# Kernel tuning notes

Measured on AMD Instinct MI355X. Metric: run time of the kernel, lower is better.

The kernel has to match this reference:

```python
import jax, jax.numpy as jnp
import numpy as np

N, E, B = 100000, 400000, 2048     # nodes, edges, graphs
H, L = 300, 5                      # hidden_feats, n_layers
NT, EF, T = 120, 16, 128           # num_node_types, in_edge_feats, n_tasks
EPS = 1e-5                         # BatchNorm eps (eval mode, running_mean=0, running_var=1)


def setup_inputs() -> dict:
    key = jax.random.key(0)
    ks = jax.random.split(key, 16)
    g = lambda i, shape, s=0.05: jax.random.normal(ks[i], shape, jnp.float32) * s
    return dict(
        node_types=jax.random.randint(ks[0], (N,), 0, NT),
        src=jax.random.randint(ks[1], (E,), 0, N),
        dst=jax.random.randint(ks[2], (E,), 0, N),
        graph_ids=jnp.sort(jax.random.randint(ks[3], (N,), 0, B)),
        edge_feats=jax.random.normal(ks[4], (E, EF), jnp.float32),
        node_emb=g(5, (NT, H), 1.0),          # nn.Embedding(num_node_types, H)
        Wn=g(6, (L, H, H)), bn=g(7, (L, H), 0.01),      # per-layer node projection
        We=g(8, (L, EF, H)), be=g(9, (L, H), 0.01),     # per-layer edge projection
        root=g(10, (L, H)),                   # per-layer root embedding (Embedding(1,H))
        gamma=1.0 + g(11, (L, H), 0.01), beta=g(12, (L, H), 0.01),  # layer BN
        vn_emb=g(13, (H,)),                   # virtual node embedding (Embedding(1,H))
        W1=g(14, (L - 1, H, 2 * H)), b1=jnp.zeros((L - 1, 2 * H), jnp.float32),
        g1=jnp.ones((L - 1, 2 * H), jnp.float32), be1=jnp.zeros((L - 1, 2 * H), jnp.float32),
        W2=g(15, (L - 1, 2 * H, H)), b2=jnp.zeros((L - 1, H), jnp.float32),
        g2=jnp.ones((L - 1, H), jnp.float32), be2=jnp.zeros((L - 1, H), jnp.float32),
        pW=jax.random.normal(jax.random.fold_in(key, 99), (H, T), jnp.float32) * 0.05,
        pb=jnp.zeros((T,), jnp.float32),
    )


def _bn(x, ga, be_):
    # eval-mode BatchNorm1d with running_mean=0, running_var=1
    return x * (ga / jnp.sqrt(1.0 + EPS)) + be_


def reference(node_types, src, dst, graph_ids, edge_feats, node_emb,
              Wn, bn, We, be, root, gamma, beta, vn_emb,
              W1, b1, g1, be1, W2, b2, g2, be2, pW, pb):
    ones_e = jnp.ones((E,), jnp.float32)
    deg = jax.ops.segment_sum(ones_e, dst, num_segments=N) + 1.0   # in_degrees + 1
    norm = deg ** -0.5
    edge_norm = (norm[src] * norm[dst])[:, None]                   # (E, 1)
    inv_deg = (1.0 / deg)[:, None]                                 # (N, 1)

    h = node_emb[node_types]                      # (N, H) node encoder
    vn = jnp.broadcast_to(vn_emb, (B, H))         # (B, H) virtual node feats

    for l in range(L):
        h = h + vn[graph_ids]                     # dgl.broadcast_nodes
        x = h @ Wn[l] + bn[l]                     # (N, H)
        e = edge_feats @ We[l] + be[l]            # (E, H)
        m = edge_norm * jax.nn.relu(x[src] + e)   # per-edge messages
        agg = jax.ops.segment_sum(m, dst, num_segments=N)          # (N, H)
        out = agg + jax.nn.relu(x + root[l]) * inv_deg
        out = _bn(out, gamma[l], beta[l])
        if l != L - 1:
            out = jax.nn.relu(out)
        h_in = h                                  # h_list[l] (after vn broadcast add)
        h = out                                   # dropout p=0 -> identity; residual=False
        if l < L - 1:
            vtmp = jax.ops.segment_sum(h_in, graph_ids, num_segments=B) + vn
            z = jax.nn.relu(_bn(vtmp @ W1[l] + b1[l], g1[l], be1[l]))
            vn = jax.nn.relu(_bn(z @ W2[l] + b2[l], g2[l], be2[l]))

    # mean readout over each graph, then linear head
    counts = jax.ops.segment_sum(jnp.ones((N,), jnp.float32), graph_ids, num_segments=B)
    gsum = jax.ops.segment_sum(h, graph_ids, num_segments=B)
    gmean = gsum / jnp.maximum(counts, 1.0)[:, None]
    return gmean @ pW + pb                        # (B, n_tasks)
```

## Files before the change

### kernel.cpp

```cpp
#include <hip/hip_runtime.h>
#include <hip/hip_bf16.h>
#include <hip/hip_fp16.h>

#define N_ 100000
#define MPAD 100096
#define E_ 400000
#define B_ 2048
#define H_ 300
#define KP_ 320
#define L_ 5
#define EF_ 16
#define T_ 128
#define ANODES 4
#define EMAX 96
#define BNS 0.9999950000374997f

typedef unsigned short ushort_t;
typedef short bf16x8 __attribute__((ext_vector_type(8)));
typedef float f32x4 __attribute__((ext_vector_type(4)));

__device__ __forceinline__ ushort_t f2b(float v) {
    unsigned u = __float_as_uint(v);
    unsigned r = (u + 0x7FFFu + ((u >> 16) & 1u)) >> 16;
    return (ushort_t)r;
}

__device__ __forceinline__ float b2f(ushort_t u) {
    return __uint_as_float(((unsigned)u) << 16);
}

__device__ __forceinline__ void gl_lds16(const void* g, void* l) {
    __builtin_amdgcn_global_load_lds(
        (const __attribute__((address_space(1))) void*)g,
        (__attribute__((address_space(3))) void*)l, 16, 0, 0);
}

__device__ __forceinline__ int swzcol(int r, int j) {
    int u = ((j >> 3) & 3) ^ ((r >> 1) & 3);
    return (j & ~31) | (u << 3) | (j & 7);
}

__global__ void k_hist(const int* __restrict__ dst, int* __restrict__ degi, int E) {
    int e = blockIdx.x * blockDim.x + threadIdx.x;
    if (e < E) atomicAdd(&degi[dst[e]], 1);
}

__global__ void k_norm(const int* __restrict__ degi, float* __restrict__ nrm,
                       float* __restrict__ invdeg, int N) {
    int n = blockIdx.x * blockDim.x + threadIdx.x;
    if (n < N) {
        float d = (float)degi[n] + 1.0f;
        nrm[n] = 1.0f / sqrtf(d);
        invdeg[n] = 1.0f / d;
    }
}

__global__ void k_scan1(const int* __restrict__ in, int* __restrict__ out,
                        int* __restrict__ partial, int N) {
    __shared__ int s[1024];
    int i = blockIdx.x * 1024 + threadIdx.x;
    int v = (i < N) ? in[i] : 0;
    s[threadIdx.x] = v;
    __syncthreads();
    for (int off = 1; off < 1024; off <<= 1) {
        int t = (threadIdx.x >= off) ? s[threadIdx.x - off] : 0;
        __syncthreads();
        s[threadIdx.x] += t;
        __syncthreads();
    }
    if (i < N) out[i] = s[threadIdx.x] - v;
    if (threadIdx.x == 1023) partial[blockIdx.x] = s[1023];
}

__global__ void k_scan2(int* __restrict__ partial, int nb, int* __restrict__ totalOut) {
    __shared__ int sh[128];
    int t = threadIdx.x;
    int v = (t < nb) ? partial[t] : 0;
    sh[t] = v;
    __syncthreads();
    for (int off = 1; off < 128; off <<= 1) {
        int u = (t >= off) ? sh[t - off] : 0;
        __syncthreads();
        sh[t] += u;
        __syncthreads();
    }
    if (t < nb) partial[t] = sh[t] - v;
    if (t == 127) *totalOut = sh[127];
}

__global__ void k_scan3(int* __restrict__ out, const int* __restrict__ partial, int N) {
    int i = blockIdx.x * 1024 + threadIdx.x;
    if (i < N) out[i] += partial[blockIdx.x];
}

__global__ void k_scatter(const int* __restrict__ dst, const int* __restrict__ src,
                          const float* __restrict__ ef, const float* __restrict__ nrm,
                          int* __restrict__ cursor, int* __restrict__ csrc_s,
                          ushort_t* __restrict__ ef16, float* __restrict__ en_csr, int E) {
    int e = blockIdx.x * blockDim.x + threadIdx.x;
    if (e >= E) return;
    int d = dst[e], s = src[e];
    int pos = atomicAdd(&cursor[d], 1);
    csrc_s[pos] = s * KP_;
    en_csr[pos] = nrm[s] * nrm[d];
    const float4* ep = (const float4*)&ef[(size_t)e * EF_];
    float4 e0 = ep[0], e1 = ep[1], e2 = ep[2], e3 = ep[3];
    uint4 ua, ub;
    ua.x = __builtin_bit_cast(unsigned, __floats2half2_rn(e0.x, e0.y));
    ua.y = __builtin_bit_cast(unsigned, __floats2half2_rn(e0.z, e0.w));
    ua.z = __builtin_bit_cast(unsigned, __floats2half2_rn(e1.x, e1.y));
    ua.w = __builtin_bit_cast(unsigned, __floats2half2_rn(e1.z, e1.w));
    ub.x = __builtin_bit_cast(unsigned, __floats2half2_rn(e2.x, e2.y));
    ub.y = __builtin_bit_cast(unsigned, __floats2half2_rn(e2.z, e2.w));
    ub.z = __builtin_bit_cast(unsigned, __floats2half2_rn(e3.x, e3.y));
    ub.w = __builtin_bit_cast(unsigned, __floats2half2_rn(e3.z, e3.w));
    uint4* op = (uint4*)&ef16[(size_t)pos * 16];
    op[0] = ua; op[1] = ub;
}

__global__ void k_rowstart(const int* __restrict__ gid, int* __restrict__ rs, int N, int B) {
    int b = blockIdx.x * blockDim.x + threadIdx.x;
    if (b <= B) {
        int lo = 0, hi = N;
        while (lo < hi) { int mid = (lo + hi) >> 1; if (gid[mid] < b) lo = mid + 1; else hi = mid; }
        rs[b] = lo;
    }
}

__global__ void k_hinit(const int* __restrict__ nt, const float* __restrict__ emb,
                        const float* __restrict__ vn_emb,
                        ushort_t* __restrict__ h_bf) {
    int n = blockIdx.x; int j = threadIdx.x;
    if (j >= KP_) return;
    float v = (j < H_) ? emb[(size_t)nt[n] * H_ + j] + vn_emb[j] : 0.f;
    h_bf[(size_t)n * KP_ + swzcol(n, j)] = f2b(v);
}

__global__ void k_vninit(const float* __restrict__ vn_emb, float* __restrict__ vn) {
    int b = blockIdx.x; int j = threadIdx.x;
    if (j >= H_) return;
    vn[(size_t)b * H_ + j] = vn_emb[j];
}

__global__ void k_convW(const float* __restrict__ W, ushort_t* __restrict__ WT,
                        int nl, int K, int Nout, int KPv, int NPBv) {
    int UPR = KPv / 8;
    int tot = nl * NPBv * UPR;
    int idx = blockIdx.x * 256 + threadIdx.x;
    if (idx >= tot) return;
    int l = idx / (NPBv * UPR); int r = idx % (NPBv * UPR);
    int n = r / UPR; int ku = r % UPR;
    int k0 = ku * 8;
    int swz = (ku & 3) ^ ((n >> 1) & 3);
    size_t d = ((size_t)l * NPBv + n) * KPv + (size_t)(k0 & ~31) + swz * 8;
    #pragma unroll
    for (int i = 0; i < 8; i++) {
        int k = k0 + i;
        float v = (k < K && n < Nout) ? W[((size_t)l * K + k) * Nout + n] : 0.f;
        WT[d + i] = f2b(v);
    }
}

__global__ void k_convWeh(const float* __restrict__ We, unsigned* __restrict__ Weh) {
    int idx = blockIdx.x * 256 + threadIdx.x;
    if (idx >= L_ * 8 * H_) return;
    int l = idx / (8 * H_); int r = idx % (8 * H_);
    int k2 = r / H_; int j = r % H_;
    float a = We[((size_t)l * EF_ + 2 * k2) * H_ + j];
    float b = We[((size_t)l * EF_ + 2 * k2 + 1) * H_ + j];
    Weh[((size_t)l * 8 + k2) * H_ + j] = __builtin_bit_cast(unsigned, __floats2half2_rn(a, b));
}

#define MB 128
#define NB 128
__launch_bounds__(256)
__global__ void k_bgemm(const ushort_t* __restrict__ A, const ushort_t* __restrict__ BT,
                        int M, int Nn, int KP,
                        const float* __restrict__ bias, const float* __restrict__ scale,
                        const float* __restrict__ shift, int relu,
                        float* __restrict__ Cf, int ldf,
                        ushort_t* __restrict__ Cb, int ldb, int swzout) {
    __shared__ ushort_t As[MB * 32];
    __shared__ ushort_t Bs[NB * 32];
    int tid = threadIdx.x;
    int lane = tid & 63, wid = tid >> 6;
    int wm = wid >> 1, wn = wid & 1;
    int m0 = blockIdx.x * MB, n0 = blockIdx.y * NB;
    f32x4 acc[4][4];
    #pragma unroll
    for (int mi = 0; mi < 4; mi++)
        #pragma unroll
        for (int ni = 0; ni < 4; ni++)
            acc[mi][ni] = (f32x4){0.f, 0.f, 0.f, 0.f};

    const ushort_t* Ab = A + (size_t)m0 * KP;
    const ushort_t* Bb = BT + (size_t)n0 * KP;
    int lr = lane & 15, lg = lane >> 4;

    for (int k0 = 0; k0 < KP; k0 += 32) {
        #pragma unroll
        for (int i = 0; i < 2; i++) {
            int li = tid + 256 * i;
            int r = li >> 2, u = li & 3;
            gl_lds16(Ab + (size_t)r * KP + k0 + u * 8, &As[(size_t)(li & ~63) * 8]);
        }
        #pragma unroll
        for (int i = 0; i < 2; i++) {
            int li = tid + 256 * i;
            int r = li >> 2, u = li & 3;
            gl_lds16(Bb + (size_t)r * KP + k0 + u * 8, &Bs[(size_t)(li & ~63) * 8]);
        }
        __syncthreads();
        bf16x8 af[4], bv[4];
        #pragma unroll
        for (int mi = 0; mi < 4; mi++) {
            int rr = wm * 64 + mi * 16 + lr;
            int uu = lg ^ ((rr >> 1) & 3);
            af[mi] = *(const bf16x8*)&As[rr * 32 + uu * 8];
        }
        #pragma unroll
        for (int ni = 0; ni < 4; ni++) {
            int rr = wn * 64 + ni * 16 + lr;
            int uu = lg ^ ((rr >> 1) & 3);
            bv[ni] = *(const bf16x8*)&Bs[rr * 32 + uu * 8];
        }
        #pragma unroll
        for (int mi = 0; mi < 4; mi++)
            #pragma unroll
            for (int ni = 0; ni < 4; ni++)
                acc[mi][ni] = __builtin_amdgcn_mfma_f32_16x16x32_bf16(
                    af[mi], bv[ni], acc[mi][ni], 0, 0, 0);
        __syncthreads();
    }

    #pragma unroll
    for (int ni = 0; ni < 4; ni++) {
        int gn = n0 + wn * 64 + ni * 16 + lr;
        if (gn >= Nn) continue;
        float bvv = bias[gn];
        float sc = scale ? scale[gn] * BNS : 0.f;
        float sh = shift ? shift[gn] : 0.f;
        #pragma unroll
        for (int mi = 0; mi < 4; mi++) {
            #pragma unroll
            for (int t = 0; t < 4; t++) {
                int gm = m0 + wm * 64 + mi * 16 + lg * 4 + t;
                if (gm >= M) continue;
                float v = acc[mi][ni][t] + bvv;
                if (scale) v = v * sc + sh;
                if (relu) v = fmaxf(v, 0.f);
                if (Cf) Cf[(size_t)gm * ldf + gn] = v;
                else    Cb[(size_t)gm * ldb + (swzout ? swzcol(gm, gn) : gn)] = f2b(v);
            }
        }
    }
}

__launch_bounds__(256)
__global__ void k_vtmp(const ushort_t* __restrict__ h_bf, const float* __restrict__ vn,
                       const int* __restrict__ rs, ushort_t* __restrict__ vtmp_bf) {
    __shared__ float red[40 * 8 * 6];
    int b = blockIdx.x;
    int t = threadIdx.x;
    int u = t % 40, rr = t / 40;
    int s = rs[b], e = rs[b + 1];
    if (rr < 6) {
        float a8[8] = {0.f, 0.f, 0.f, 0.f, 0.f, 0.f, 0.f, 0.f};
        int g = u >> 2, w = u & 3;
        for (int n = s + rr; n < e; n += 6) {
            int phys = (g << 2) | (w ^ ((n >> 1) & 3));
            bf16x8 hv = *(const bf16x8*)&h_bf[(size_t)n * KP_ + phys * 8];
            #pragma unroll
            for (int k = 0; k < 8; k++) a8[k] += b2f((ushort_t)hv[k]);
        }
        #pragma unroll
        for (int k = 0; k < 8; k++) red[(u * 8 + k) * 6 + rr] = a8[k];
    }
    __syncthreads();
    if (t < 40) {
        int g = t >> 2, w = t & 3;
        int phys = (g << 2) | (w ^ ((b >> 1) & 3));
        ushort_t ov[8];
        #pragma unroll
        for (int k = 0; k < 8; k++) {
            int j = t * 8 + k;
            float sum = 0.f;
            #pragma unroll
            for (int r = 0; r < 6; r++) sum += red[(t * 8 + k) * 6 + r];
            float val = (j < H_) ? sum + vn[(size_t)b * H_ + j] : 0.f;
            ov[k] = f2b(val);
        }
        *(bf16x8*)&vtmp_bf[(size_t)b * KP_ + phys * 8] = *(bf16x8*)ov;
    }
}

__launch_bounds__(256)
__global__ void k_readout(const ushort_t* __restrict__ h_bf, const int* __restrict__ rs,
                          const float* __restrict__ pW, const float* __restrict__ pb,
                          float* __restrict__ out) {
    __shared__ float red[40 * 8 * 6];
    __shared__ float gg[320];
    int b = blockIdx.x;
    int t = threadIdx.x;
    int u = t % 40, rr = t / 40;
    int s = rs[b], e = rs[b + 1];
    if (rr < 6) {
        float a8[8] = {0.f, 0.f, 0.f, 0.f, 0.f, 0.f, 0.f, 0.f};
        int g = u >> 2, w = u & 3;
        for (int n = s + rr; n < e; n += 6) {
            int phys = (g << 2) | (w ^ ((n >> 1) & 3));
            bf16x8 hv = *(const bf16x8*)&h_bf[(size_t)n * KP_ + phys * 8];
            #pragma unroll
            for (int k = 0; k < 8; k++) a8[k] += b2f((ushort_t)hv[k]);
        }
        #pragma unroll
        for (int k = 0; k < 8; k++) red[(u * 8 + k) * 6 + rr] = a8[k];
    }
    __syncthreads();
    if (t < 40) {
        int cnt = e - s; if (cnt < 1) cnt = 1;
        float ic = 1.f / (float)cnt;
        #pragma unroll
        for (int k = 0; k < 8; k++) {
            float sum = 0.f;
            #pragma unroll
            for (int r = 0; r < 6; r++) sum += red[(t * 8 + k) * 6 + r];
            gg[t * 8 + k] = sum * ic;
        }
    }
    __syncthreads();
    if (t < T_) {
        float o = pb[t];
        #pragma unroll 4
        for (int k = 0; k < H_; k++) o = fmaf(gg[k], pW[(size_t)k * T_ + t], o);
        out[(size_t)b * T_ + t] = o;
    }
}

__device__ __forceinline__ float eproj8(const uint4& ea, const uint4& eb,
                                        const __half2* wh, float bej) {
    __half2 hs = __floats2half2_rn(0.f, 0.f);
    hs = __hfma2(__builtin_bit_cast(__half2, ea.x), wh[0], hs);
    hs = __hfma2(__builtin_bit_cast(__half2, ea.y), wh[1], hs);
    hs = __hfma2(__builtin_bit_cast(__half2, ea.z), wh[2], hs);
    hs = __hfma2(__builtin_bit_cast(__half2, ea.w), wh[3], hs);
    hs = __hfma2(__builtin_bit_cast(__half2, eb.x), wh[4], hs);
    hs = __hfma2(__builtin_bit_cast(__half2, eb.y), wh[5], hs);
    hs = __hfma2(__builtin_bit_cast(__half2, eb.z), wh[6], hs);
    hs = __hfma2(__builtin_bit_cast(__half2, eb.w), wh[7], hs);
    return bej + __low2float(hs) + __high2float(hs);
}

__launch_bounds__(320)
__global__ void k_agg(const ushort_t* __restrict__ x_bf,
                      ushort_t* __restrict__ h_bf,
                      const int* __restrict__ off, const int* __restrict__ csrc_s,
                      const ushort_t* __restrict__ ef16, const float* __restrict__ en_csr,
                      const unsigned* __restrict__ Weh_l, const float* __restrict__ be_l,
                      const float* __restrict__ invdeg,
                      const float* __restrict__ root_l, const float* __restrict__ gamma_l,
                      const float* __restrict__ beta_l,
                      const float* __restrict__ vn_next, const int* __restrict__ gid,
                      int relu) {
    __shared__ int s_src[EMAX];
    __shared__ float s_en[EMAX];
    __shared__ unsigned s_ef[EMAX * 8];
    int n0 = blockIdx.x * ANODES;
    int tid = threadIdx.x;
    int j = tid;

    int o0 = off[n0], o1 = off[n0 + 1], o2 = off[n0 + 2],
        o3 = off[n0 + 3], o4 = off[n0 + 4];
    int estart = o0, cnt = o4 - o0;
    bool lds_ok = cnt <= EMAX;

    if (lds_ok) {
        const unsigned* efu = (const unsigned*)ef16;
        for (int t = tid; t < cnt; t += 320) {
            s_src[t] = csrc_s[estart + t];
            s_en[t] = en_csr[estart + t];
        }
        for (int uu = tid; uu < 8 * cnt; uu += 320)
            s_ef[uu] = efu[(size_t)estart * 8 + uu];
    }
    __syncthreads();

    if (j >= H_) return;
    __half2 wh[8];
    #pragma unroll
    for (int k2 = 0; k2 < 8; k2++)
        wh[k2] = __builtin_bit_cast(__half2, Weh_l[k2 * H_ + j]);
    float bej = be_l[j];

    float xn[ANODES];
    #pragma unroll
    for (int ln = 0; ln < ANODES; ln++)
        xn[ln] = b2f(x_bf[(size_t)(n0 + ln) * KP_ + j]);

    int re[ANODES] = {o1 - o0, o2 - o0, o3 - o0, o4 - o0};
    float accv[ANODES];
    int rel = 0;
    #pragma unroll
    for (int ln = 0; ln < ANODES; ln++) {
        int rend = re[ln];
        float a = 0.f;
        for (int q = rel; q < rend; q += 4) {
            int i0 = q;
            int i1 = (q + 1 < rend) ? q + 1 : rend - 1;
            int i2 = (q + 2 < rend) ? q + 2 : rend - 1;
            int i3 = (q + 3 < rend) ? q + 3 : rend - 1;
            int s0 = lds_ok ? s_src[i0] : csrc_s[estart + i0];
            int s1 = lds_ok ? s_src[i1] : csrc_s[estart + i1];
            int s2 = lds_ok ? s_src[i2] : csrc_s[estart + i2];
            int s3 = lds_ok ? s_src[i3] : csrc_s[estart + i3];
            float en0 = lds_ok ? s_en[i0] : en_csr[estart + i0];
            float en1 = (q + 1 < rend) ? (lds_ok ? s_en[i1] : en_csr[estart + i1]) : 0.f;
            float en2 = (q + 2 < rend) ? (lds_ok ? s_en[i2] : en_csr[estart + i2]) : 0.f;
            float en3 = (q + 3 < rend) ? (lds_ok ? s_en[i3] : en_csr[estart + i3]) : 0.f;
            float xv0 = b2f(x_bf[(size_t)s0 + j]);
            float xv1 = b2f(x_bf[(size_t)s1 + j]);
            float xv2 = b2f(x_bf[(size_t)s2 + j]);
            float xv3 = b2f(x_bf[(size_t)s3 + j]);
            uint4 a0, b0, a1, b1, a2, b2, a3, b3;
            if (lds_ok) {
                a0 = *(const uint4*)&s_ef[i0 * 8]; b0 = *(const uint4*)&s_ef[i0 * 8 + 4];
                a1 = *(const uint4*)&s_ef[i1 * 8]; b1 = *(const uint4*)&s_ef[i1 * 8 + 4];
                a2 = *(const uint4*)&s_ef[i2 * 8]; b2 = *(const uint4*)&s_ef[i2 * 8 + 4];
                a3 = *(const uint4*)&s_ef[i3 * 8]; b3 = *(const uint4*)&s_ef[i3 * 8 + 4];
            } else {
                const uint4* p0 = (const uint4*)&ef16[(size_t)(estart + i0) * 16];
                const uint4* p1 = (const uint4*)&ef16[(size_t)(estart + i1) * 16];
                const uint4* p2 = (const uint4*)&ef16[(size_t)(estart + i2) * 16];
                const uint4* p3 = (const uint4*)&ef16[(size_t)(estart + i3) * 16];
                a0 = p0[0]; b0 = p0[1]; a1 = p1[0]; b1 = p1[1];
                a2 = p2[0]; b2 = p2[1]; a3 = p3[0]; b3 = p3[1];
            }
            a = fmaf(en0, fmaxf(xv0 + eproj8(a0, b0, wh, bej), 0.f), a);
            a = fmaf(en1, fmaxf(xv1 + eproj8(a1, b1, wh, bej), 0.f), a);
            a = fmaf(en2, fmaxf(xv2 + eproj8(a2, b2, wh, bej), 0.f), a);
            a = fmaf(en3, fmaxf(xv3 + eproj8(a3, b3, wh, bej), 0.f), a);
        }
        accv[ln] = a;
        rel = rend;
    }

    float rootj = root_l[j], gmj = gamma_l[j] * BNS, btj = beta_l[j];
    #pragma unroll
    for (int ln = 0; ln < ANODES; ln++) {
        int n = n0 + ln;
        float v = accv[ln] + fmaxf(xn[ln] + rootj, 0.f) * invdeg[n];
        v = v * gmj + btj;
        if (relu) v = fmaxf(v, 0.f);
        if (vn_next) v += vn_next[(size_t)gid[n] * H_ + j];
        h_bf[(size_t)n * KP_ + swzcol(n, j)] = f2b(v);
    }
}

extern "C" void kernel_launch(void* const* d_in, const int* in_sizes, int n_in,
                              void* d_out, int out_size, void* d_ws, size_t ws_size,
                              hipStream_t stream) {
    const int* node_types = (const int*)d_in[0];
    const int* src        = (const int*)d_in[1];
    const int* dst        = (const int*)d_in[2];
    const int* graph_ids  = (const int*)d_in[3];
    const float* edge_feats = (const float*)d_in[4];
    const float* node_emb   = (const float*)d_in[5];
    const float* Wn   = (const float*)d_in[6];
    const float* bn   = (const float*)d_in[7];
    const float* We   = (const float*)d_in[8];
    const float* be   = (const float*)d_in[9];
    const float* root = (const float*)d_in[10];
    const float* gamma = (const float*)d_in[11];
    const float* beta  = (const float*)d_in[12];
    const float* vn_emb = (const float*)d_in[13];
    const float* W1  = (const float*)d_in[14];
    const float* b1  = (const float*)d_in[15];
    const float* g1  = (const float*)d_in[16];
    const float* be1 = (const float*)d_in[17];
    const float* W2  = (const float*)d_in[18];
    const float* b2  = (const float*)d_in[19];
    const float* g2  = (const float*)d_in[20];
    const float* be2 = (const float*)d_in[21];
    const float* pW  = (const float*)d_in[22];
    const float* pb  = (const float*)d_in[23];
    float* out = (float*)d_out;

    char* p = (char*)d_ws;
    auto alloc = [&](size_t bytes) { void* q = (void*)p; p += (bytes + 255) & ~(size_t)255; return q; };
    ushort_t* h_bf   = (ushort_t*)alloc((size_t)MPAD * KP_ * 2);
    ushort_t* x_bf   = (ushort_t*)alloc((size_t)MPAD * KP_ * 2);
    ushort_t* ef16   = (ushort_t*)alloc((size_t)E_ * 16 * 2);
    ushort_t* WnT    = (ushort_t*)alloc((size_t)L_ * 384 * KP_ * 2);
    unsigned* Weh    = (unsigned*)alloc((size_t)L_ * 8 * H_ * 4);
    ushort_t* W1T    = (ushort_t*)alloc((size_t)4 * 640 * KP_ * 2);
    ushort_t* W2T    = (ushort_t*)alloc((size_t)4 * 384 * 640 * 2);
    ushort_t* vtmp_bf= (ushort_t*)alloc((size_t)B_ * KP_ * 2);
    ushort_t* z_bf   = (ushort_t*)alloc((size_t)B_ * 640 * 2);
    float* vn    = (float*)alloc((size_t)B_ * H_ * 4);
    float* nrm   = (float*)alloc((size_t)N_ * 4);
    float* invdeg= (float*)alloc((size_t)N_ * 4);
    int* degi    = (int*)alloc((size_t)N_ * 4);
    int* csr_off = (int*)alloc((size_t)(N_ + 1) * 4);
    int* cursor  = (int*)alloc((size_t)N_ * 4);
    int* csrc_s  = (int*)alloc((size_t)E_ * 4);
    float* en_csr= (float*)alloc((size_t)E_ * 4);
    int* rs      = (int*)alloc((size_t)(B_ + 1) * 4);
    int* partial = (int*)alloc((size_t)128 * 4);

    const int SCAN_NB = (N_ + 1023) / 1024;

    hipMemsetAsync(degi, 0, (size_t)N_ * 4, stream);
    k_hist<<<(E_ + 255) / 256, 256, 0, stream>>>(dst, degi, E_);
    k_norm<<<(N_ + 255) / 256, 256, 0, stream>>>(degi, nrm, invdeg, N_);

    k_scan1<<<SCAN_NB, 1024, 0, stream>>>(degi, csr_off, partial, N_);
    k_scan2<<<1, 128, 0, stream>>>(partial, SCAN_NB, csr_off + N_);
    k_scan3<<<SCAN_NB, 1024, 0, stream>>>(csr_off, partial, N_);
    hipMemcpyAsync(cursor, csr_off, (size_t)N_ * 4, hipMemcpyDeviceToDevice, stream);
    k_scatter<<<(E_ + 255) / 256, 256, 0, stream>>>(dst, src, edge_feats, nrm,
                                                    cursor, csrc_s, ef16, en_csr, E_);

    k_rowstart<<<(B_ + 1 + 255) / 256, 256, 0, stream>>>(graph_ids, rs, N_, B_);

    k_convW<<<(L_ * 384 * (KP_ / 8) + 255) / 256, 256, 0, stream>>>(Wn, WnT, L_, H_, H_, KP_, 384);
    k_convWeh<<<(L_ * 8 * H_ + 255) / 256, 256, 0, stream>>>(We, Weh);
    k_convW<<<(4 * 640 * (KP_ / 8) + 255) / 256, 256, 0, stream>>>(W1, W1T, 4, H_, 2 * H_, KP_, 640);
    k_convW<<<(4 * 384 * (640 / 8) + 255) / 256, 256, 0, stream>>>(W2, W2T, 4, 2 * H_, H_, 640, 384);

    k_hinit<<<N_, 320, 0, stream>>>(node_types, node_emb, vn_emb, h_bf);
    k_vninit<<<B_, 320, 0, stream>>>(vn_emb, vn);

    dim3 gx(MPAD / MB, 3);
    dim3 gz(B_ / MB, 5);
    dim3 gv(B_ / MB, 3);

    for (int l = 0; l < L_; l++) {
        k_bgemm<<<gx, 256, 0, stream>>>(h_bf, WnT + (size_t)l * 384 * KP_,
                                        N_, H_, KP_,
                                        bn + (size_t)l * H_, nullptr, nullptr, 0,
                                        nullptr, 0, x_bf, KP_, 0);
        if (l < L_ - 1) {
            k_vtmp<<<B_, 256, 0, stream>>>(h_bf, vn, rs, vtmp_bf);
            k_bgemm<<<gz, 256, 0, stream>>>(vtmp_bf, W1T + (size_t)l * 640 * KP_,
                                            B_, 2 * H_, KP_,
                                            b1 + (size_t)l * 2 * H_,
                                            g1 + (size_t)l * 2 * H_, be1 + (size_t)l * 2 * H_, 1,
                                            nullptr, 0, z_bf, 640, 1);
            k_bgemm<<<gv, 256, 0, stream>>>(z_bf, W2T + (size_t)l * 384 * 640,
                                            B_, H_, 640,
                                            b2 + (size_t)l * H_,
                                            g2 + (size_t)l * H_, be2 + (size_t)l * H_, 1,
                                            vn, H_, nullptr, 0, 0);
        }
        k_agg<<<N_ / ANODES, 320, 0, stream>>>(x_bf, h_bf, csr_off, csrc_s,
                                               ef16, en_csr,
                                               Weh + (size_t)l * 8 * H_, be + (size_t)l * H_,
                                               invdeg,
                                               root + (size_t)l * H_,
                                               gamma + (size_t)l * H_, beta + (size_t)l * H_,
                                               (l < L_ - 1) ? vn : nullptr, graph_ids,
                                               (l < L_ - 1) ? 1 : 0);
    }

    k_readout<<<B_, 256, 0, stream>>>(h_bf, rs, pW, pb, out);
}
```

Measured before the change: 1.794 ms.

## Pack edge metadata, use fdot2 edge projection, widen aggregation to 8 nodes

Merges the per-edge source offset and normalization into one int2 array, so the aggregation kernel does one 8-byte load per edge instead of two 4-byte loads. Replaces the half2 FMA chain in the edge projection with fdot2 instructions that accumulate in fp32. Doubles the nodes per block to 8 and raises the LDS edge capacity to 128, which halves the block count and amortizes the per-block weight loads. Fewer blocks may cut occupancy, and more blocks may exceed the LDS capacity and take the slower global fallback.

New measurement: 1.772 ms. About the same (-1.3%).

```diff
diff --git a/kernel.cpp b/kernel.cpp
--- a/kernel.cpp
+++ b/kernel.cpp
@@ -11,13 +11,14 @@
 #define L_ 5
 #define EF_ 16
 #define T_ 128
-#define ANODES 4
-#define EMAX 96
+#define ANODES 8
+#define EMAX 128
 #define BNS 0.9999950000374997f
 
 typedef unsigned short ushort_t;
 typedef short bf16x8 __attribute__((ext_vector_type(8)));
 typedef float f32x4 __attribute__((ext_vector_type(4)));
+typedef _Float16 h2f __attribute__((ext_vector_type(2)));
 
 __device__ __forceinline__ ushort_t f2b(float v) {
     unsigned u = __float_as_uint(v);
@@ -95,14 +96,16 @@
 
 __global__ void k_scatter(const int* __restrict__ dst, const int* __restrict__ src,
                           const float* __restrict__ ef, const float* __restrict__ nrm,
-                          int* __restrict__ cursor, int* __restrict__ csrc_s,
-                          ushort_t* __restrict__ ef16, float* __restrict__ en_csr, int E) {
+                          int* __restrict__ cursor, int2* __restrict__ meta,
+                          ushort_t* __restrict__ ef16, int E) {
     int e = blockIdx.x * blockDim.x + threadIdx.x;
     if (e >= E) return;
     int d = dst[e], s = src[e];
     int pos = atomicAdd(&cursor[d], 1);
-    csrc_s[pos] = s * KP_;
-    en_csr[pos] = nrm[s] * nrm[d];
+    int2 md;
+    md.x = s * KP_;
+    md.y = __float_as_int(nrm[s] * nrm[d]);
+    meta[pos] = md;
     const float4* ep = (const float4*)&ef[(size_t)e * EF_];
     float4 e0 = ep[0], e1 = ep[1], e2 = ep[2], e3 = ep[3];
     uint4 ua, ub;
@@ -337,59 +340,56 @@
     }
 }
 
-__device__ __forceinline__ float eproj8(const uint4& ea, const uint4& eb,
-                                        const __half2* wh, float bej) {
-    __half2 hs = __floats2half2_rn(0.f, 0.f);
-    hs = __hfma2(__builtin_bit_cast(__half2, ea.x), wh[0], hs);
-    hs = __hfma2(__builtin_bit_cast(__half2, ea.y), wh[1], hs);
-    hs = __hfma2(__builtin_bit_cast(__half2, ea.z), wh[2], hs);
-    hs = __hfma2(__builtin_bit_cast(__half2, ea.w), wh[3], hs);
-    hs = __hfma2(__builtin_bit_cast(__half2, eb.x), wh[4], hs);
-    hs = __hfma2(__builtin_bit_cast(__half2, eb.y), wh[5], hs);
-    hs = __hfma2(__builtin_bit_cast(__half2, eb.z), wh[6], hs);
-    hs = __hfma2(__builtin_bit_cast(__half2, eb.w), wh[7], hs);
-    return bej + __low2float(hs) + __high2float(hs);
+__device__ __forceinline__ float eproj8d(const uint4& ea, const uint4& eb,
+                                         const h2f* wh, float bej) {
+    float ev = bej;
+    ev = __builtin_amdgcn_fdot2(__builtin_bit_cast(h2f, ea.x), wh[0], ev, false);
+    ev = __builtin_amdgcn_fdot2(__builtin_bit_cast(h2f, ea.y), wh[1], ev, false);
+    ev = __builtin_amdgcn_fdot2(__builtin_bit_cast(h2f, ea.z), wh[2], ev, false);
+    ev = __builtin_amdgcn_fdot2(__builtin_bit_cast(h2f, ea.w), wh[3], ev, false);
+    ev = __builtin_amdgcn_fdot2(__builtin_bit_cast(h2f, eb.x), wh[4], ev, false);
+    ev = __builtin_amdgcn_fdot2(__builtin_bit_cast(h2f, eb.y), wh[5], ev, false);
+    ev = __builtin_amdgcn_fdot2(__builtin_bit_cast(h2f, eb.z), wh[6], ev, false);
+    ev = __builtin_amdgcn_fdot2(__builtin_bit_cast(h2f, eb.w), wh[7], ev, false);
+    return ev;
 }
 
 __launch_bounds__(320)
 __global__ void k_agg(const ushort_t* __restrict__ x_bf,
                       ushort_t* __restrict__ h_bf,
-                      const int* __restrict__ off, const int* __restrict__ csrc_s,
-                      const ushort_t* __restrict__ ef16, const float* __restrict__ en_csr,
+                      const int* __restrict__ off, const int2* __restrict__ meta,
+                      const ushort_t* __restrict__ ef16,
                       const unsigned* __restrict__ Weh_l, const float* __restrict__ be_l,
                       const float* __restrict__ invdeg,
                       const float* __restrict__ root_l, const float* __restrict__ gamma_l,
                       const float* __restrict__ beta_l,
                       const float* __restrict__ vn_next, const int* __restrict__ gid,
                       int relu) {
-    __shared__ int s_src[EMAX];
-    __shared__ float s_en[EMAX];
+    __shared__ int2 s_md[EMAX];
     __shared__ unsigned s_ef[EMAX * 8];
     int n0 = blockIdx.x * ANODES;
     int tid = threadIdx.x;
     int j = tid;
 
-    int o0 = off[n0], o1 = off[n0 + 1], o2 = off[n0 + 2],
-        o3 = off[n0 + 3], o4 = off[n0 + 4];
-    int estart = o0, cnt = o4 - o0;
+    int offv[ANODES + 1];
+    #pragma unroll
+    for (int k = 0; k <= ANODES; k++) offv[k] = off[n0 + k];
+    int estart = offv[0], cnt = offv[ANODES] - estart;
     bool lds_ok = cnt <= EMAX;
 
     if (lds_ok) {
         const unsigned* efu = (const unsigned*)ef16;
-        for (int t = tid; t < cnt; t += 320) {
-            s_src[t] = csrc_s[estart + t];
-            s_en[t] = en_csr[estart + t];
-        }
+        for (int t = tid; t < cnt; t += 320) s_md[t] = meta[estart + t];
         for (int uu = tid; uu < 8 * cnt; uu += 320)
             s_ef[uu] = efu[(size_t)estart * 8 + uu];
     }
     __syncthreads();
 
     if (j >= H_) return;
-    __half2 wh[8];
+    h2f wh[8];
     #pragma unroll
     for (int k2 = 0; k2 < 8; k2++)
-        wh[k2] = __builtin_bit_cast(__half2, Weh_l[k2 * H_ + j]);
+        wh[k2] = __builtin_bit_cast(h2f, Weh_l[k2 * H_ + j]);
     float bej = be_l[j];
 
     float xn[ANODES];
@@ -397,30 +397,28 @@
     for (int ln = 0; ln < ANODES; ln++)
         xn[ln] = b2f(x_bf[(size_t)(n0 + ln) * KP_ + j]);
 
-    int re[ANODES] = {o1 - o0, o2 - o0, o3 - o0, o4 - o0};
     float accv[ANODES];
-    int rel = 0;
     #pragma unroll
     for (int ln = 0; ln < ANODES; ln++) {
-        int rend = re[ln];
+        int rel = offv[ln] - estart, rend = offv[ln + 1] - estart;
         float a = 0.f;
         for (int q = rel; q < rend; q += 4) {
             int i0 = q;
             int i1 = (q + 1 < rend) ? q + 1 : rend - 1;
             int i2 = (q + 2 < rend) ? q + 2 : rend - 1;
             int i3 = (q + 3 < rend) ? q + 3 : rend - 1;
-            int s0 = lds_ok ? s_src[i0] : csrc_s[estart + i0];
-            int s1 = lds_ok ? s_src[i1] : csrc_s[estart + i1];
-            int s2 = lds_ok ? s_src[i2] : csrc_s[estart + i2];
-            int s3 = lds_ok ? s_src[i3] : csrc_s[estart + i3];
-            float en0 = lds_ok ? s_en[i0] : en_csr[estart + i0];
-            float en1 = (q + 1 < rend) ? (lds_ok ? s_en[i1] : en_csr[estart + i1]) : 0.f;
-            float en2 = (q + 2 < rend) ? (lds_ok ? s_en[i2] : en_csr[estart + i2]) : 0.f;
-            float en3 = (q + 3 < rend) ? (lds_ok ? s_en[i3] : en_csr[estart + i3]) : 0.f;
-            float xv0 = b2f(x_bf[(size_t)s0 + j]);
-            float xv1 = b2f(x_bf[(size_t)s1 + j]);
-            float xv2 = b2f(x_bf[(size_t)s2 + j]);
-            float xv3 = b2f(x_bf[(size_t)s3 + j]);
+            int2 m0 = lds_ok ? s_md[i0] : meta[estart + i0];
+            int2 m1 = lds_ok ? s_md[i1] : meta[estart + i1];
+            int2 m2 = lds_ok ? s_md[i2] : meta[estart + i2];
+            int2 m3 = lds_ok ? s_md[i3] : meta[estart + i3];
+            float en0 = __int_as_float(m0.y);
+            float en1 = (q + 1 < rend) ? __int_as_float(m1.y) : 0.f;
+            float en2 = (q + 2 < rend) ? __int_as_float(m2.y) : 0.f;
+            float en3 = (q + 3 < rend) ? __int_as_float(m3.y) : 0.f;
+            float xv0 = b2f(x_bf[(size_t)m0.x + j]);
+            float xv1 = b2f(x_bf[(size_t)m1.x + j]);
+            float xv2 = b2f(x_bf[(size_t)m2.x + j]);
+            float xv3 = b2f(x_bf[(size_t)m3.x + j]);
             uint4 a0, b0, a1, b1, a2, b2, a3, b3;
             if (lds_ok) {
                 a0 = *(const uint4*)&s_ef[i0 * 8]; b0 = *(const uint4*)&s_ef[i0 * 8 + 4];
@@ -435,13 +433,12 @@
                 a0 = p0[0]; b0 = p0[1]; a1 = p1[0]; b1 = p1[1];
                 a2 = p2[0]; b2 = p2[1]; a3 = p3[0]; b3 = p3[1];
             }
-            a = fmaf(en0, fmaxf(xv0 + eproj8(a0, b0, wh, bej), 0.f), a);
-            a = fmaf(en1, fmaxf(xv1 + eproj8(a1, b1, wh, bej), 0.f), a);
-            a = fmaf(en2, fmaxf(xv2 + eproj8(a2, b2, wh, bej), 0.f), a);
-            a = fmaf(en3, fmaxf(xv3 + eproj8(a3, b3, wh, bej), 0.f), a);
+            a = fmaf(en0, fmaxf(xv0 + eproj8d(a0, b0, wh, bej), 0.f), a);
+            a = fmaf(en1, fmaxf(xv1 + eproj8d(a1, b1, wh, bej), 0.f), a);
+            a = fmaf(en2, fmaxf(xv2 + eproj8d(a2, b2, wh, bej), 0.f), a);
+            a = fmaf(en3, fmaxf(xv3 + eproj8d(a3, b3, wh, bej), 0.f), a);
         }
         accv[ln] = a;
-        rel = rend;
     }
 
     float rootj = root_l[j], gmj = gamma_l[j] * BNS, btj = beta_l[j];
@@ -502,8 +499,7 @@
     int* degi    = (int*)alloc((size_t)N_ * 4);
     int* csr_off = (int*)alloc((size_t)(N_ + 1) * 4);
     int* cursor  = (int*)alloc((size_t)N_ * 4);
-    int* csrc_s  = (int*)alloc((size_t)E_ * 4);
-    float* en_csr= (float*)alloc((size_t)E_ * 4);
+    int2* meta   = (int2*)alloc((size_t)E_ * 8);
     int* rs      = (int*)alloc((size_t)(B_ + 1) * 4);
     int* partial = (int*)alloc((size_t)128 * 4);
 
@@ -518,7 +514,7 @@
     k_scan3<<<SCAN_NB, 1024, 0, stream>>>(csr_off, partial, N_);
     hipMemcpyAsync(cursor, csr_off, (size_t)N_ * 4, hipMemcpyDeviceToDevice, stream);
     k_scatter<<<(E_ + 255) / 256, 256, 0, stream>>>(dst, src, edge_feats, nrm,
-                                                    cursor, csrc_s, ef16, en_csr, E_);
+                                                    cursor, meta, ef16, E_);
 
     k_rowstart<<<(B_ + 1 + 255) / 256, 256, 0, stream>>>(graph_ids, rs, N_, B_);
 
@@ -552,8 +548,7 @@
                                             g2 + (size_t)l * H_, be2 + (size_t)l * H_, 1,
                                             vn, H_, nullptr, 0, 0);
         }
-        k_agg<<<N_ / ANODES, 320, 0, stream>>>(x_bf, h_bf, csr_off, csrc_s,
-                                               ef16, en_csr,
+        k_agg<<<N_ / ANODES, 320, 0, stream>>>(x_bf, h_bf, csr_off, meta, ef16,
                                                Weh + (size_t)l * 8 * H_, be + (size_t)l * H_,
                                                invdeg,
                                                root + (size_t)l * H_,
```
